# Kernel optimization log

Hardware: AMD Instinct MI355X
Metric: run time of the kernel (lower is better)

The kernel has to match this reference:

```python
import jax, jax.numpy as jnp
import numpy as np
from jax import lax

# ---- config (matches init_kwargs) ----
B, T, H = 4, 2048, 1024
HU = 4 * H                 # h_up = hidden*4
LAYERS, INDEX = 12, 0
K_CLAMP, K_EPS = 60.0, 1e-8
LN_EPS = 1e-5


def setup_inputs() -> dict:
    key = jax.random.key(0)
    ks = jax.random.split(key, 9)
    s = 0.02  # weight scale
    tr01 = INDEX / (LAYERS - 1)          # time_ratio_0_to_1
    tr1pz = 1.0 - INDEX / LAYERS         # time_ratio_1_to_pz
    i_h = np.arange(H, dtype=np.float64) / H
    i_hu = np.arange(HU, dtype=np.float64)
    # per-channel decay speed / first (sized to the WKV channel dim h_up)
    decay_speed = -5.0 + 8.0 * (i_hu / (HU - 1)) ** (0.7 + 1.3 * tr01)
    zigzag = ((np.arange(HU) + 1) % 3 - 1) * 0.5
    time_first = np.log(0.3) + zigzag
    f32 = lambda a: jnp.asarray(a, jnp.float32)
    return {
        "x": jax.random.normal(ks[0], (B, T, H), jnp.float32),
        "ln0_g": jnp.ones((H,), jnp.float32), "ln0_b": jnp.zeros((H,), jnp.float32),
        "pre_g": jnp.ones((H,), jnp.float32), "pre_b": jnp.zeros((H,), jnp.float32),
        "post_g": jnp.ones((H,), jnp.float32), "post_b": jnp.zeros((H,), jnp.float32),
        "tm_decay": f32(decay_speed),
        "tm_first": f32(time_first),
        "tm_mix_k": f32(i_h ** tr1pz),
        "tm_mix_v": f32(i_h ** tr1pz + 0.3 * tr01),
        "tm_mix_r": f32(i_h ** (0.5 * tr1pz)),
        "tm_Wk": jax.random.normal(ks[1], (H, HU), jnp.float32) * s,
        "tm_Wv": jax.random.normal(ks[2], (H, HU), jnp.float32) * s,
        "tm_Wr": jax.random.normal(ks[3], (H, HU), jnp.float32) * s,
        "tm_Wo": jax.random.normal(ks[4], (HU, H), jnp.float32) * s,
        "cm_mix_k": f32(i_h ** tr1pz),
        "cm_mix_r": f32(i_h ** tr1pz),
        "cm_Wk": jax.random.normal(ks[5], (H, HU), jnp.float32) * s,
        "cm_Wv": jax.random.normal(ks[6], (HU, H), jnp.float32) * s,
        "cm_Wr": jax.random.normal(ks[7], (H, H), jnp.float32) * s,
    }


def _ln(x, g, b):
    m = jnp.mean(x, -1, keepdims=True)
    v = jnp.mean((x - m) ** 2, -1, keepdims=True)
    return (x - m) / jnp.sqrt(v + LN_EPS) * g + b


def _shift(x):  # ZeroPad2d((0,0,1,-1)): xx[:, t] = x[:, t-1], xx[:, 0] = 0
    return jnp.pad(x[:, :-1], ((0, 0), (1, 0), (0, 0)))


def _wkv(k, kv, decay, first):
    # k, kv: [B, T, HU]; decay, first: [HU]
    # wkv[t] = first*kv[t] + sum_{d>=1} decay^(d-1) * kv[t-d]  (same for k)
    def step(carry, inp):
        sk, skv = carry
        kt, kvt = inp
        out = (first * kt + sk, first * kvt + skv)
        return (kt + decay * sk, kvt + decay * skv), out
    b = k.shape[0]
    init = (jnp.zeros((b, k.shape[2]), k.dtype), jnp.zeros((b, k.shape[2]), k.dtype))
    _, (wk, wkv) = lax.scan(step, init, (jnp.swapaxes(k, 0, 1), jnp.swapaxes(kv, 0, 1)))
    return jnp.swapaxes(wk, 0, 1), jnp.swapaxes(wkv, 0, 1)


def reference(x, ln0_g, ln0_b, pre_g, pre_b, post_g, post_b,
              tm_decay, tm_first, tm_mix_k, tm_mix_v, tm_mix_r,
              tm_Wk, tm_Wv, tm_Wr, tm_Wo,
              cm_mix_k, cm_mix_r, cm_Wk, cm_Wv, cm_Wr):
    if INDEX == 0:
        x = _ln(x, ln0_g, ln0_b)

    # ---- RWKV_TM (time mix / WKV) ----
    xn = _ln(x, pre_g, pre_b)
    xx = _shift(xn)
    xk = xn * tm_mix_k + xx * (1.0 - tm_mix_k)
    xv = xn * tm_mix_v + xx * (1.0 - tm_mix_v)
    xr = xn * tm_mix_r + xx * (1.0 - tm_mix_r)
    k = jnp.exp(jnp.minimum(xk @ tm_Wk, K_CLAMP))   # [B,T,HU]
    v = xv @ tm_Wv                                  # [B,T,HU]
    r = xr @ tm_Wr                                  # [B,T,HU]
    kv = k * v
    decay = jnp.exp(-jnp.exp(tm_decay))  # per-step multiplier exp(-exp(time_decay))
    first = jnp.exp(tm_first)
    wk, wkv = _wkv(k, kv, decay, first)
    rwkv = jax.nn.sigmoid(r) * (wkv / (wk + K_EPS))
    x = x + rwkv @ tm_Wo

    # ---- RWKV_CM (channel mix) ----
    xn = _ln(x, post_g, post_b)
    xx = _shift(xn)
    xk = xn * cm_mix_k + xx * (1.0 - cm_mix_k)
    xr = xn * cm_mix_r + xx * (1.0 - cm_mix_r)
    kv = jax.nn.silu(xk @ cm_Wk) @ cm_Wv            # [B,T,H]
    x = x + (jax.nn.sigmoid(xr @ cm_Wr) + kv)
    return x
```

## Files before the change

kernel.cpp:

```cpp
#include <hip/hip_runtime.h>

#define Hdim  1024
#define Tdim  2048
#define Bdim  4
#define HUdim 4096
#define Mrows (Bdim*Tdim)
#define CHUNK 2048
#define NCH   (HUdim/CHUNK)
#define NSEG  16
#define SEGL  (Tdim/NSEG)
#define SCHUNK 16

typedef __bf16 bf16;
typedef __bf16 bf16x2 __attribute__((ext_vector_type(2)));
typedef __bf16 bf16x8 __attribute__((ext_vector_type(8)));
typedef float  floatx4 __attribute__((ext_vector_type(4)));

__device__ __forceinline__ bf16 f2bf(float x) { return (bf16)x; }

__global__ __launch_bounds__(256) void wconv_all(
    const float* __restrict__ s0, const float* __restrict__ s1, const float* __restrict__ s2,
    const float* __restrict__ s3, const float* __restrict__ s4, const float* __restrict__ s5,
    const float* __restrict__ s6,
    bf16* d0, bf16* d1, bf16* d2, bf16* d3, bf16* d4, bf16* d5, bf16* d6) {
  __shared__ float tile[64][65];
  int bid = blockIdx.x;
  const float* src; bf16* dst; int K, N, local;
  if (bid < 1024)      { src = s0; dst = d0; K = Hdim;  N = HUdim; local = bid; }
  else if (bid < 2048) { src = s1; dst = d1; K = Hdim;  N = HUdim; local = bid - 1024; }
  else if (bid < 3072) { src = s2; dst = d2; K = Hdim;  N = HUdim; local = bid - 2048; }
  else if (bid < 4096) { src = s3; dst = d3; K = HUdim; N = Hdim;  local = bid - 3072; }
  else if (bid < 5120) { src = s4; dst = d4; K = Hdim;  N = HUdim; local = bid - 4096; }
  else if (bid < 6144) { src = s5; dst = d5; K = HUdim; N = Hdim;  local = bid - 5120; }
  else                 { src = s6; dst = d6; K = Hdim;  N = Hdim;  local = bid - 6144; }
  const int nt = N >> 6;
  const int n0 = (local % nt) * 64, k0 = (local / nt) * 64;
  const int tr = threadIdx.x >> 6;
  const int tc = threadIdx.x & 63;
#pragma unroll
  for (int j = 0; j < 16; j++) {
    int r = j * 4 + tr;
    tile[r][tc] = src[(size_t)(k0 + r) * N + n0 + tc];
  }
  __syncthreads();
#pragma unroll
  for (int j = 0; j < 16; j++) {
    int r = j * 4 + tr;
    dst[(size_t)(n0 + r) * K + k0 + tc] = f2bf(tile[tc][r]);
  }
}

__device__ __forceinline__ void block_reduce4(float v[4], float* sm) {
#pragma unroll
  for (int off = 32; off > 0; off >>= 1) {
#pragma unroll
    for (int i = 0; i < 4; i++) v[i] += __shfl_down(v[i], off, 64);
  }
  const int w = threadIdx.x >> 6;
  if ((threadIdx.x & 63) == 0) {
#pragma unroll
    for (int i = 0; i < 4; i++) sm[w * 4 + i] = v[i];
  }
  __syncthreads();
#pragma unroll
  for (int i = 0; i < 4; i++) v[i] = sm[i] + sm[4 + i] + sm[8 + i] + sm[12 + i];
  __syncthreads();
}

__global__ __launch_bounds__(256) void ln_mix_tm(
    const float* __restrict__ x,
    const float* __restrict__ g0, const float* __restrict__ b0,
    const float* __restrict__ g1, const float* __restrict__ b1,
    const float* __restrict__ mk, const float* __restrict__ mv, const float* __restrict__ mr,
    float* __restrict__ x0, bf16* __restrict__ xk, bf16* __restrict__ xv, bf16* __restrict__ xr) {
  __shared__ float sm[16];
  const int bid = blockIdx.x;
  const int t = bid & (Tdim - 1);
  const int tid = threadIdx.x;
  const bool havep = (t > 0);
  const float hp = havep ? 1.f : 0.f;
  const float* rowc = x + (size_t)bid * Hdim;
  const float* rowp = havep ? (rowc - Hdim) : rowc;

  float c[4], p[4];
#pragma unroll
  for (int j = 0; j < 4; j++) c[j] = rowc[tid * 4 + j];
#pragma unroll
  for (int j = 0; j < 4; j++) p[j] = rowp[tid * 4 + j] * hp;

  float red[4] = {0.f, 0.f, 0.f, 0.f};
#pragma unroll
  for (int j = 0; j < 4; j++) { red[0] += c[j]; red[1] += c[j]*c[j]; red[2] += p[j]; red[3] += p[j]*p[j]; }
  block_reduce4(red, sm);
  const float inv = 1.f / Hdim;
  float mc = red[0]*inv, vc = red[1]*inv - mc*mc;
  float mp = red[2]*inv, vp = red[3]*inv - mp*mp;
  float sc = rsqrtf(vc + 1e-5f), sp = rsqrtf(vp + 1e-5f);

  float yc[4], yp[4];
#pragma unroll
  for (int j = 0; j < 4; j++) {
    int i = tid * 4 + j;
    yc[j] = (c[j] - mc) * sc * g0[i] + b0[i];
    yp[j] = ((p[j] - mp) * sp * g0[i] + b0[i]) * hp;
    x0[(size_t)bid * Hdim + i] = yc[j];
  }

  float r2[4] = {0.f, 0.f, 0.f, 0.f};
#pragma unroll
  for (int j = 0; j < 4; j++) { r2[0] += yc[j]; r2[1] += yc[j]*yc[j]; r2[2] += yp[j]; r2[3] += yp[j]*yp[j]; }
  block_reduce4(r2, sm);
  float mc2 = r2[0]*inv, vc2 = r2[1]*inv - mc2*mc2;
  float mp2 = r2[2]*inv, vp2 = r2[3]*inv - mp2*mp2;
  float sc2 = rsqrtf(vc2 + 1e-5f), sp2 = rsqrtf(vp2 + 1e-5f);

#pragma unroll
  for (int j = 0; j < 4; j++) {
    int i = tid * 4 + j;
    float xnc = (yc[j] - mc2) * sc2 * g1[i] + b1[i];
    float xnp = ((yp[j] - mp2) * sp2 * g1[i] + b1[i]) * hp;
    size_t o = (size_t)bid * Hdim + i;
    float a;
    a = mk[i]; xk[o] = f2bf(xnc * a + xnp * (1.f - a));
    a = mv[i]; xv[o] = f2bf(xnc * a + xnp * (1.f - a));
    a = mr[i]; xr[o] = f2bf(xnc * a + xnp * (1.f - a));
  }
}

__global__ __launch_bounds__(256) void ln_mix_cm(
    const float* __restrict__ xin,
    const float* __restrict__ g, const float* __restrict__ bb,
    const float* __restrict__ mk, const float* __restrict__ mr,
    bf16* __restrict__ xk, bf16* __restrict__ xr) {
  __shared__ float sm[16];
  const int bid = blockIdx.x;
  const int t = bid & (Tdim - 1);
  const int tid = threadIdx.x;
  const bool havep = (t > 0);
  const float hp = havep ? 1.f : 0.f;
  const float* rowc = xin + (size_t)bid * Hdim;
  const float* rowp = havep ? (rowc - Hdim) : rowc;

  float c[4], p[4];
#pragma unroll
  for (int j = 0; j < 4; j++) c[j] = rowc[tid * 4 + j];
#pragma unroll
  for (int j = 0; j < 4; j++) p[j] = rowp[tid * 4 + j] * hp;

  float red[4] = {0.f, 0.f, 0.f, 0.f};
#pragma unroll
  for (int j = 0; j < 4; j++) { red[0] += c[j]; red[1] += c[j]*c[j]; red[2] += p[j]; red[3] += p[j]*p[j]; }
  block_reduce4(red, sm);
  const float inv = 1.f / Hdim;
  float mc = red[0]*inv, vc = red[1]*inv - mc*mc;
  float mp = red[2]*inv, vp = red[3]*inv - mp*mp;
  float sc = rsqrtf(vc + 1e-5f), sp = rsqrtf(vp + 1e-5f);

#pragma unroll
  for (int j = 0; j < 4; j++) {
    int i = tid * 4 + j;
    float xnc = (c[j] - mc) * sc * g[i] + bb[i];
    float xnp = ((p[j] - mp) * sp * g[i] + bb[i]) * hp;
    size_t o = (size_t)bid * Hdim + i;
    float a;
    a = mk[i]; xk[o] = f2bf(xnc * a + xnp * (1.f - a));
    a = mr[i]; xr[o] = f2bf(xnc * a + xnp * (1.f - a));
  }
}

__global__ __launch_bounds__(64) void wkv_part(
    const bf16* __restrict__ Kb, const bf16* __restrict__ Vb,
    float* __restrict__ stK, float* __restrict__ stKV,
    const float* __restrict__ tdec) {
  const int seg = blockIdx.x & (NSEG - 1);
  const int rest = blockIdx.x >> 4;
  const int b = rest >> 4, g = rest & 15;
  const int c = (g << 7) + (threadIdx.x << 1);
  const float d0 = __expf(-__expf(tdec[c]));
  const float d1 = __expf(-__expf(tdec[c + 1]));
  size_t base = ((size_t)b * Tdim + (size_t)seg * SEGL) * CHUNK + c;
  float sk0 = 0.f, skv0 = 0.f, sk1 = 0.f, skv1 = 0.f;
  for (int t0 = 0; t0 < SEGL; t0 += SCHUNK) {
    bf16x2 kk[SCHUNK], vv[SCHUNK];
#pragma unroll
    for (int j = 0; j < SCHUNK; j++) {
      size_t idx = base + (size_t)(t0 + j) * CHUNK;
      kk[j] = *(const bf16x2*)(Kb + idx);
      vv[j] = *(const bf16x2*)(Vb + idx);
    }
#pragma unroll
    for (int j = 0; j < SCHUNK; j++) {
      float k0 = (float)kk[j][0], k1 = (float)kk[j][1];
      float v0 = (float)vv[j][0], v1 = (float)vv[j][1];
      sk0  = fmaf(d0, sk0, k0);   skv0 = fmaf(d0, skv0, k0 * v0);
      sk1  = fmaf(d1, sk1, k1);   skv1 = fmaf(d1, skv1, k1 * v1);
    }
  }
  size_t so = ((size_t)seg * Bdim + b) * CHUNK + c;
  stK[so]      = sk0;  stK[so + 1]  = sk1;
  stKV[so]     = skv0; stKV[so + 1] = skv1;
}

__global__ __launch_bounds__(64) void wkv_emit(
    const bf16* __restrict__ Kb, const bf16* __restrict__ Vb,
    const bf16* SRb, bf16* Pb,
    const float* __restrict__ stK, const float* __restrict__ stKV,
    const float* __restrict__ tdec, const float* __restrict__ tfst) {
  const int seg = blockIdx.x & (NSEG - 1);
  const int rest = blockIdx.x >> 4;
  const int b = rest >> 4, g = rest & 15;
  const int c = (g << 7) + (threadIdx.x << 1);
  const float ed0 = __expf(tdec[c]),     ed1 = __expf(tdec[c + 1]);
  const float d0  = __expf(-ed0),        d1  = __expf(-ed1);
  const float df0 = __expf(-ed0 * (float)SEGL);
  const float df1 = __expf(-ed1 * (float)SEGL);
  const float f0  = __expf(tfst[c]),     f1  = __expf(tfst[c + 1]);

  float sk0 = 0.f, skv0 = 0.f, sk1 = 0.f, skv1 = 0.f;
  for (int j = 0; j < seg; j++) {
    size_t so = ((size_t)j * Bdim + b) * CHUNK + c;
    sk0  = fmaf(df0, sk0,  stK[so]);      sk1  = fmaf(df1, sk1,  stK[so + 1]);
    skv0 = fmaf(df0, skv0, stKV[so]);     skv1 = fmaf(df1, skv1, stKV[so + 1]);
  }

  size_t base = ((size_t)b * Tdim + (size_t)seg * SEGL) * CHUNK + c;
  for (int t0 = 0; t0 < SEGL; t0 += SCHUNK) {
    bf16x2 kk[SCHUNK], vv[SCHUNK], rr[SCHUNK];
#pragma unroll
    for (int j = 0; j < SCHUNK; j++) {
      size_t idx = base + (size_t)(t0 + j) * CHUNK;
      kk[j] = *(const bf16x2*)(Kb + idx);
      vv[j] = *(const bf16x2*)(Vb + idx);
      rr[j] = *(const bf16x2*)(SRb + idx);
    }
#pragma unroll
    for (int j = 0; j < SCHUNK; j++) {
      size_t idx = base + (size_t)(t0 + j) * CHUNK;
      float k0 = (float)kk[j][0], k1 = (float)kk[j][1];
      float v0 = (float)vv[j][0], v1 = (float)vv[j][1];
      float kv0 = k0 * v0, kv1 = k1 * v1;
      float wk0  = fmaf(f0, k0, sk0) + 1e-8f;
      float wk1  = fmaf(f1, k1, sk1) + 1e-8f;
      float wkv0 = fmaf(f0, kv0, skv0);
      float wkv1 = fmaf(f1, kv1, skv1);
      bf16x2 out;
      out[0] = f2bf((float)rr[j][0] * wkv0 * __builtin_amdgcn_rcpf(wk0));
      out[1] = f2bf((float)rr[j][1] * wkv1 * __builtin_amdgcn_rcpf(wk1));
      *(bf16x2*)(Pb + idx) = out;
      sk0  = fmaf(d0, sk0, k0);   skv0 = fmaf(d0, skv0, kv0);
      sk1  = fmaf(d1, sk1, k1);   skv1 = fmaf(d1, skv1, kv1);
    }
  }
}

__device__ __forceinline__ void gld_lds(const bf16* g, bf16* l) {
  __builtin_amdgcn_global_load_lds(
      (const __attribute__((address_space(1))) void*)(g),
      (__attribute__((address_space(3))) void*)(l),
      16, 0, 0);
}

__device__ __forceinline__ void swz(int s, int gm, int& m_t, int& n_t) {
  const int mpx  = gm >> 3;
  const int xcd  = s & 7;
  const int ss   = s >> 3;
  const int pass = mpx << 1;
  const int ng   = ss / pass;
  const int rem  = ss - ng * pass;
  m_t = xcd * mpx + (rem >> 1);
  n_t = (ng << 1) + (rem & 1);
}

__device__ __forceinline__ void mm_core64(
    const bf16* A, const bf16* Bt, int lda, int ldb, int K,
    long m0, long n0, int wv, int lane, int wm, int wn,
    bf16* As, bf16* Bs, floatx4 acc[4][4]) {
  const int srow = wv * 32 + (lane >> 2);
  const int scol = (((lane & 3) - ((lane >> 3) & 3)) & 3) * 8;
  const bf16* gA = A + (m0 + srow) * (long)lda + scol;
  const bf16* gB = Bt + (n0 + srow) * (long)ldb + scol;
  const long skipA = 16L * lda;
  const long skipB = 16L * ldb;
  bf16* lA = As + wv * 1024;
  bf16* lB = Bs + wv * 1024;
  const int pg = ((lane >> 4) + ((lane >> 1) & 3)) & 3;
  const bf16* fa = As + ((wm * 64) + (lane & 15)) * 32 + pg * 8;
  const bf16* fb = Bs + ((wn * 64) + (lane & 15)) * 32 + pg * 8;

  const int ksteps = K >> 6;
  for (int kt = 0; kt < ksteps; ++kt) {
    __syncthreads();
    gld_lds(gA, lA);             gld_lds(gA + skipA, lA + 512);
    gld_lds(gA + 32, lA + 4096); gld_lds(gA + 32 + skipA, lA + 4096 + 512);
    gld_lds(gB, lB);             gld_lds(gB + skipB, lB + 512);
    gld_lds(gB + 32, lB + 4096); gld_lds(gB + 32 + skipB, lB + 4096 + 512);
    gA += 64; gB += 64;
    __syncthreads();
#pragma unroll
    for (int s = 0; s < 2; s++) {
      bf16x8 af[4], bfr[4];
#pragma unroll
      for (int i = 0; i < 4; i++) {
        af[i]  = *(const bf16x8*)(fa + s * 4096 + i * 512);
        bfr[i] = *(const bf16x8*)(fb + s * 4096 + i * 512);
      }
#pragma unroll
      for (int mt = 0; mt < 4; mt++)
#pragma unroll
        for (int nt = 0; nt < 4; nt++)
          acc[mt][nt] = __builtin_amdgcn_mfma_f32_16x16x32_bf16(af[mt], bfr[nt], acc[mt][nt], 0, 0, 0);
    }
  }
}

enum { E_EXP = 0, E_BF16 = 1, E_SIG = 2, E_ADD1 = 3, E_SILU = 4, E_F32 = 5, E_SIGADD2 = 6 };

template <int EPI>
__device__ __forceinline__ void epilogue(
    floatx4 acc[4][4], void* Cout, const void* aux1, const void* aux2,
    long m0, long n0, int ldc, int lane, int wm, int wn) {
  const int r0 = wm * 64 + ((lane >> 4) << 2);
  const int c0 = wn * 64 + (lane & 15);
#pragma unroll
  for (int mt = 0; mt < 4; mt++) {
#pragma unroll
    for (int i = 0; i < 4; i++) {
      long r = m0 + r0 + mt * 16 + i;
      long bidx = r * (long)ldc + n0 + c0;
#pragma unroll
      for (int nt = 0; nt < 4; nt++) {
        long idx = bidx + nt * 16;
        float v = acc[mt][nt][i];
        if constexpr (EPI == E_EXP) {
          ((bf16*)Cout)[idx] = f2bf(__expf(fminf(v, 60.f)));
        } else if constexpr (EPI == E_BF16) {
          ((bf16*)Cout)[idx] = f2bf(v);
        } else if constexpr (EPI == E_SIG) {
          ((bf16*)Cout)[idx] = f2bf(1.f / (1.f + __expf(-v)));
        } else if constexpr (EPI == E_ADD1) {
          float prev = ((const float*)aux1)[idx];
          ((float*)Cout)[idx] = v + prev;
        } else if constexpr (EPI == E_SILU) {
          ((bf16*)Cout)[idx] = f2bf(v / (1.f + __expf(-v)));
        } else if constexpr (EPI == E_F32) {
          ((float*)Cout)[idx] = v;
        } else {
          float a1 = ((const float*)aux1)[idx];
          float a2 = ((const float*)aux2)[idx];
          ((float*)Cout)[idx] = a1 + 1.f / (1.f + __expf(-v)) + a2;
        }
      }
    }
  }
}

template <int EPI, int MT>
__global__ __launch_bounds__(256) void gemm_bt(
    const bf16* __restrict__ A, const bf16* __restrict__ Bt,
    void* Cout, const void* aux1, const void* aux2,
    int lda, int ldb, int ldc, int K, int gm, int gn) {
  __shared__ __align__(16) bf16 As[2 * 128 * 32];
  __shared__ __align__(16) bf16 Bs[2 * 128 * 32];
  const int tid = threadIdx.x;
  const int lane = tid & 63;
  const int wv = tid >> 6;
  const int wm = wv >> 1, wn = wv & 1;
  int m_t, n_t;
  swz(blockIdx.x, gm, m_t, n_t);
  const long n0 = (long)n_t * 128;

#pragma unroll
  for (int sm = 0; sm < MT; sm++) {
    const long m0 = (long)m_t * (128 * MT) + sm * 128;
    floatx4 acc[4][4];
#pragma unroll
    for (int i = 0; i < 4; i++)
#pragma unroll
      for (int j = 0; j < 4; j++) acc[i][j] = (floatx4){0.f, 0.f, 0.f, 0.f};
    mm_core64(A, Bt, lda, ldb, K, m0, n0, wv, lane, wm, wn, As, Bs, acc);
    epilogue<EPI>(acc, Cout, aux1, aux2, m0, n0, ldc, lane, wm, wn);
  }
}

__device__ __forceinline__ void mm_core256(
    const bf16* __restrict__ A, const bf16* __restrict__ Bt,
    int lda, int ldb, int K, long m0, long n0,
    int wv, int lane, bf16* Lds, floatx4 acc[8][4]) {
  const int wm = wv >> 2, wn = wv & 3;
  const int rA0 = wm * 128 + (wv & 3) * 16;
  const int rB0 = (wv >> 1) * 64 + (wv & 1) * 16;
  const int rl  = lane >> 2;
  const int scol = (((lane & 3) - ((lane >> 3) & 3)) & 3) * 8;
  const bf16* gA = A + (m0 + rA0 + rl) * (long)lda + scol;
  const bf16* gB = Bt + (n0 + rB0 + rl) * (long)ldb + scol;
  bf16* lA = Lds + rA0 * 32;
  bf16* lB = Lds + 16384 + rB0 * 32;

  const int pg = ((lane >> 4) + ((lane >> 1) & 3)) & 3;
  const bf16* fa0 = Lds + (wm * 128 + (lane & 15)) * 32 + pg * 8;
  const bf16* fb0 = Lds + 16384 + (wn * 64 + (lane & 15)) * 32 + pg * 8;

#define STGA8(buf, h, kt) do { \
    const bf16* _s = gA + (long)(h) * 64 * lda + (kt) * 64; \
    bf16* _d = lA + (buf) * 32768 + (h) * 2048; \
    gld_lds(_s, _d); gld_lds(_s + 32, _d + 8192); } while (0)
#define STGB8(buf, h, kt) do { \
    const bf16* _s = gB + (long)(h) * 32 * ldb + (kt) * 64; \
    bf16* _d = lB + (buf) * 32768 + (h) * 1024; \
    gld_lds(_s, _d); gld_lds(_s + 32, _d + 8192); } while (0)

  STGA8(0, 0, 0); STGB8(0, 0, 0); STGB8(0, 1, 0); STGA8(0, 1, 0);
  STGA8(1, 0, 1); STGB8(1, 0, 1); STGB8(1, 1, 1);
  asm volatile("s_waitcnt vmcnt(10)" ::: "memory");
  __builtin_amdgcn_s_barrier();

  const int niter = K >> 7;
  bf16x8 a[4][2];
  bf16x8 b[2][2][2];
  for (int it = 0; it < niter; ++it) {
    const int kt0 = it << 1;
    const bool notlast = (it != niter - 1);
#pragma unroll
    for (int ph = 0; ph < 8; ++ph) {
      const int q   = ph & 3;
      const int buf = ph >> 2;
      const int mq  = q >> 1;
      const int nq  = (q >> 1) ^ (q & 1);
      const bf16* fa = fa0 + buf * 32768 + mq * 2048;
      const bf16* fb = fb0 + buf * 32768 + nq * 1024;
      if (q == 0) {
#pragma unroll
        for (int mf = 0; mf < 4; ++mf) {
          a[mf][0] = *(const bf16x8*)(fa + mf * 512);
          a[mf][1] = *(const bf16x8*)(fa + mf * 512 + 8192);
        }
#pragma unroll
        for (int nf = 0; nf < 2; ++nf) {
          b[0][nf][0] = *(const bf16x8*)(fb + nf * 512);
          b[0][nf][1] = *(const bf16x8*)(fb + nf * 512 + 8192);
        }
      } else if (q == 1) {
#pragma unroll
        for (int nf = 0; nf < 2; ++nf) {
          b[1][nf][0] = *(const bf16x8*)(fb + nf * 512);
          b[1][nf][1] = *(const bf16x8*)(fb + nf * 512 + 8192);
        }
      } else if (q == 2) {
#pragma unroll
        for (int mf = 0; mf < 4; ++mf) {
          a[mf][0] = *(const bf16x8*)(fa + mf * 512);
          a[mf][1] = *(const bf16x8*)(fa + mf * 512 + 8192);
        }
      }
      __builtin_amdgcn_sched_barrier(0);
      if (ph == 0)            STGA8(1, 1, kt0 + 1);
      else if (notlast) {
        if (ph == 1)      STGA8(0, 0, kt0 + 2);
        else if (ph == 2) STGB8(0, 0, kt0 + 2);
        else if (ph == 3) STGB8(0, 1, kt0 + 2);
        else if (ph == 4) STGA8(0, 1, kt0 + 2);
        else if (ph == 5) STGA8(1, 0, kt0 + 3);
        else if (ph == 6) STGB8(1, 0, kt0 + 3);
        else              STGB8(1, 1, kt0 + 3);
      }
      if (notlast) {
        if (ph == 0 || ph == 1 || ph == 4 || ph == 5)
          asm volatile("s_waitcnt vmcnt(10)" ::: "memory");
        else if (ph == 3 || ph == 7)
          asm volatile("s_waitcnt vmcnt(12)" ::: "memory");
      } else {
        if (ph == 0)      asm volatile("s_waitcnt vmcnt(10)" ::: "memory");
        else if (ph == 1) asm volatile("s_waitcnt vmcnt(0)" ::: "memory");
      }
      if (q != 3) {
        __builtin_amdgcn_s_barrier();
        asm volatile("s_waitcnt lgkmcnt(0)" ::: "memory");
      }
      __builtin_amdgcn_s_setprio(1);
#pragma unroll
      for (int mf = 0; mf < 4; ++mf)
#pragma unroll
        for (int nf = 0; nf < 2; ++nf) {
          acc[mq*4+mf][nq*2+nf] = __builtin_amdgcn_mfma_f32_16x16x32_bf16(
              a[mf][0], b[nq][nf][0], acc[mq*4+mf][nq*2+nf], 0, 0, 0);
          acc[mq*4+mf][nq*2+nf] = __builtin_amdgcn_mfma_f32_16x16x32_bf16(
              a[mf][1], b[nq][nf][1], acc[mq*4+mf][nq*2+nf], 0, 0, 0);
        }
      __builtin_amdgcn_s_setprio(0);
      __builtin_amdgcn_s_barrier();
    }
  }
#undef STGA8
#undef STGB8
}

template <int EPI>
__global__ __launch_bounds__(512, 2) void gemm8(
    const bf16* __restrict__ A, const bf16* __restrict__ Bt,
    void* Cout, const void* aux1, const void* aux2,
    int lda, int ldb, int ldc, int K, int gm, int gn) {
  __shared__ __align__(16) bf16 Lds[65536];
  const int tid = threadIdx.x;
  const int lane = tid & 63;
  const int wv = tid >> 6;
  int m_t, n_t;
  swz(blockIdx.x, gm, m_t, n_t);
  const long m0 = (long)m_t * 256, n0 = (long)n_t * 256;
  floatx4 acc[8][4];
#pragma unroll
  for (int i = 0; i < 8; i++)
#pragma unroll
    for (int j = 0; j < 4; j++) acc[i][j] = (floatx4){0.f, 0.f, 0.f, 0.f};
  mm_core256(A, Bt, lda, ldb, K, m0, n0, wv, lane, Lds, acc);

  const int wm = wv >> 2, wn = wv & 3;
  const int r0 = wm * 128 + ((lane >> 4) << 2);
  const int c0 = wn * 64 + (lane & 15);
#pragma unroll
  for (int mf = 0; mf < 8; ++mf) {
#pragma unroll
    for (int i = 0; i < 4; ++i) {
      long r = m0 + r0 + mf * 16 + i;
      long bidx = r * (long)ldc + n0 + c0;
#pragma unroll
      for (int nf = 0; nf < 4; ++nf) {
        long idx = bidx + nf * 16;
        float v = acc[mf][nf][i];
        if constexpr (EPI == E_SILU) {
          ((bf16*)Cout)[idx] = f2bf(v / (1.f + __expf(-v)));
        } else if constexpr (EPI == E_BF16) {
          ((bf16*)Cout)[idx] = f2bf(v);
        } else if constexpr (EPI == E_F32) {
          ((float*)Cout)[idx] = v;
        } else if constexpr (EPI == E_ADD1) {
          float prev = ((const float*)aux1)[idx];
          ((float*)Cout)[idx] = v + prev;
        }
      }
    }
  }
}

__global__ __launch_bounds__(512, 2) void proj8(
    const bf16* __restrict__ xk, const bf16* __restrict__ xv, const bf16* __restrict__ xr,
    const bf16* __restrict__ Wk, const bf16* __restrict__ Wv, const bf16* __restrict__ Wr,
    bf16* Kc, bf16* Vc, bf16* SRc, int gm, int gn) {
  __shared__ __align__(16) bf16 Lds[65536];
  const int per = gm * gn;
  const int sub = blockIdx.x / per;
  const int s   = blockIdx.x - sub * per;
  const int tid = threadIdx.x;
  const int lane = tid & 63;
  const int wv = tid >> 6;
  int m_t, n_t;
  swz(s, gm, m_t, n_t);
  const long m0 = (long)m_t * 256, n0 = (long)n_t * 256;

  const bf16* A  = (sub == 0) ? xk : (sub == 1) ? xv : xr;
  const bf16* Bt = (sub == 0) ? Wk : (sub == 1) ? Wv : Wr;
  bf16*       C  = (sub == 0) ? Kc : (sub == 1) ? Vc : SRc;

  floatx4 acc[8][4];
#pragma unroll
  for (int i = 0; i < 8; i++)
#pragma unroll
    for (int j = 0; j < 4; j++) acc[i][j] = (floatx4){0.f, 0.f, 0.f, 0.f};
  mm_core256(A, Bt, Hdim, Hdim, Hdim, m0, n0, wv, lane, Lds, acc);

  const int wm = wv >> 2, wn = wv & 3;
  const int r0 = wm * 128 + ((lane >> 4) << 2);
  const int c0 = wn * 64 + (lane & 15);
#pragma unroll
  for (int mf = 0; mf < 8; ++mf) {
#pragma unroll
    for (int i = 0; i < 4; ++i) {
      long r = m0 + r0 + mf * 16 + i;
      long bidx = r * (long)CHUNK + n0 + c0;
#pragma unroll
      for (int nf = 0; nf < 4; ++nf) {
        long idx = bidx + nf * 16;
        float v = acc[mf][nf][i];
        float o;
        if (sub == 0)      o = __expf(fminf(v, 60.f));
        else if (sub == 1) o = v;
        else               o = 1.f / (1.f + __expf(-v));
        C[idx] = f2bf(o);
      }
    }
  }
}

extern "C" void kernel_launch(void* const* d_in, const int* in_sizes, int n_in,
                              void* d_out, int out_size, void* d_ws, size_t ws_size,
                              hipStream_t stream) {
  (void)in_sizes; (void)n_in; (void)out_size; (void)ws_size;
  const float* x        = (const float*)d_in[0];
  const float* ln0_g    = (const float*)d_in[1];
  const float* ln0_b    = (const float*)d_in[2];
  const float* pre_g    = (const float*)d_in[3];
  const float* pre_b    = (const float*)d_in[4];
  const float* post_g   = (const float*)d_in[5];
  const float* post_b   = (const float*)d_in[6];
  const float* tm_decay = (const float*)d_in[7];
  const float* tm_first = (const float*)d_in[8];
  const float* tm_mix_k = (const float*)d_in[9];
  const float* tm_mix_v = (const float*)d_in[10];
  const float* tm_mix_r = (const float*)d_in[11];
  const float* tm_Wk    = (const float*)d_in[12];
  const float* tm_Wv    = (const float*)d_in[13];
  const float* tm_Wr    = (const float*)d_in[14];
  const float* tm_Wo    = (const float*)d_in[15];
  const float* cm_mix_k = (const float*)d_in[16];
  const float* cm_mix_r = (const float*)d_in[17];
  const float* cm_Wk    = (const float*)d_in[18];
  const float* cm_Wv    = (const float*)d_in[19];
  const float* cm_Wr    = (const float*)d_in[20];

  char* ws = (char*)d_ws;
  bf16*  WkT  = (bf16*)(ws + 0);
  bf16*  WvT  = (bf16*)(ws + 8388608);
  bf16*  WrT  = (bf16*)(ws + 16777216);
  bf16*  WoT  = (bf16*)(ws + 25165824);
  bf16*  cWkT = (bf16*)(ws + 33554432);
  bf16*  cWvT = (bf16*)(ws + 41943040);
  bf16*  cWrT = (bf16*)(ws + 50331648);
  float* xres = (float*)(ws + 52428800);
  bf16*  xk   = (bf16*)(ws + 85983232);
  bf16*  xv   = (bf16*)(ws + 102760448);
  bf16*  xr   = (bf16*)(ws + 119537664);
  bf16*  Kc   = (bf16*)(ws + 136314880);
  bf16*  Vc   = (bf16*)(ws + 169869312);
  bf16*  SRc  = (bf16*)(ws + 203423744);
  float* stK  = (float*)(ws + 236978176);
  float* stKV = (float*)(ws + 237502464);
  bf16*  xk2  = (bf16*)(ws + 136314880);
  bf16*  xr2  = (bf16*)(ws + 153092096);
  bf16*  hbuf = (bf16*)(ws + 169869312);
  float* hv   = (float*)(ws + 85983232);

  dim3 blk(256);
  wconv_all<<<6400, blk, 0, stream>>>(tm_Wk, tm_Wv, tm_Wr, tm_Wo, cm_Wk, cm_Wv, cm_Wr,
                                      WkT, WvT, WrT, WoT, cWkT, cWvT, cWrT);

  ln_mix_tm<<<Mrows, blk, 0, stream>>>(x, ln0_g, ln0_b, pre_g, pre_b,
                                       tm_mix_k, tm_mix_v, tm_mix_r, xres, xk, xv, xr);

  const int scan_grid = NSEG * Bdim * (CHUNK / 128);
  const int GM = Mrows / 128;
  const int GM8 = Mrows / 256;
  const int GN8p = CHUNK / 256;
  for (int ch = 0; ch < NCH; ch++) {
    const long woff = (long)ch * CHUNK;
    proj8<<<3 * GM8 * GN8p, dim3(512), 0, stream>>>(
        xk, xv, xr, WkT + woff * Hdim, WvT + woff * Hdim, WrT + woff * Hdim,
        Kc, Vc, SRc, GM8, GN8p);

    wkv_part<<<scan_grid, dim3(64), 0, stream>>>(
        Kc, Vc, stK, stKV, tm_decay + woff);
    wkv_emit<<<scan_grid, dim3(64), 0, stream>>>(
        Kc, Vc, SRc, SRc, stK, stKV, tm_decay + woff, tm_first + woff);

    gemm_bt<E_ADD1, 1><<<GM * (Hdim/128), blk, 0, stream>>>(
        SRc, WoT + woff, xres, xres, nullptr, CHUNK, HUdim, Hdim, CHUNK, GM, Hdim/128);
  }

  ln_mix_cm<<<Mrows, blk, 0, stream>>>(xres, post_g, post_b, cm_mix_k, cm_mix_r, xk2, xr2);

  gemm8<E_SILU><<<GM8 * (HUdim/256), dim3(512), 0, stream>>>(
      xk2, cWkT, hbuf, nullptr, nullptr, Hdim, Hdim, HUdim, Hdim, GM8, HUdim/256);

  gemm_bt<E_F32, 1><<<GM * (Hdim/128), blk, 0, stream>>>(
      hbuf, cWvT, hv, nullptr, nullptr, HUdim, HUdim, Hdim, CHUNK, GM, Hdim/128);
  gemm_bt<E_ADD1, 1><<<GM * (Hdim/128), blk, 0, stream>>>(
      hbuf + CHUNK, cWvT + CHUNK, hv, hv, nullptr, HUdim, HUdim, Hdim, CHUNK, GM, Hdim/128);

  gemm_bt<E_SIGADD2, 1><<<GM * (Hdim/128), blk, 0, stream>>>(
      xr2, cWrT, (float*)d_out, xres, hv, Hdim, Hdim, Hdim, Hdim, GM, Hdim/128);
}
```

Before: 959.6 us.

## Replace 128x128 GEMMs with triple-buffered 256x128 pipelined kernel for N=1024 outputs

Replaces the single-buffered 128x128 gemm_bt kernel, which synchronizes twice per k-step, with a 512-thread 256x128 tile kernel. The new kernel triple-buffers LDS, prefetches two k-steps ahead with direct global-to-LDS loads, and raises wave priority during MFMA bursts. It also merges the two split-K cm_Wv GEMMs into one full-K launch, dropping an fp32 read-modify-write pass over hv. It uses far more LDS per block (144KB), which limits occupancy, and the grid is halved to 256 blocks for the N=1024 GEMMs.

```diff
diff --git a/kernel.cpp b/kernel.cpp
--- a/kernel.cpp
+++ b/kernel.cpp
@@ -269,48 +269,6 @@
   const int rem  = ss - ng * pass;
   m_t = xcd * mpx + (rem >> 1);
   n_t = (ng << 1) + (rem & 1);
-}
-
-__device__ __forceinline__ void mm_core64(
-    const bf16* A, const bf16* Bt, int lda, int ldb, int K,
-    long m0, long n0, int wv, int lane, int wm, int wn,
-    bf16* As, bf16* Bs, floatx4 acc[4][4]) {
-  const int srow = wv * 32 + (lane >> 2);
-  const int scol = (((lane & 3) - ((lane >> 3) & 3)) & 3) * 8;
-  const bf16* gA = A + (m0 + srow) * (long)lda + scol;
-  const bf16* gB = Bt + (n0 + srow) * (long)ldb + scol;
-  const long skipA = 16L * lda;
-  const long skipB = 16L * ldb;
-  bf16* lA = As + wv * 1024;
-  bf16* lB = Bs + wv * 1024;
-  const int pg = ((lane >> 4) + ((lane >> 1) & 3)) & 3;
-  const bf16* fa = As + ((wm * 64) + (lane & 15)) * 32 + pg * 8;
-  const bf16* fb = Bs + ((wn * 64) + (lane & 15)) * 32 + pg * 8;
-
-  const int ksteps = K >> 6;
-  for (int kt = 0; kt < ksteps; ++kt) {
-    __syncthreads();
-    gld_lds(gA, lA);             gld_lds(gA + skipA, lA + 512);
-    gld_lds(gA + 32, lA + 4096); gld_lds(gA + 32 + skipA, lA + 4096 + 512);
-    gld_lds(gB, lB);             gld_lds(gB + skipB, lB + 512);
-    gld_lds(gB + 32, lB + 4096); gld_lds(gB + 32 + skipB, lB + 4096 + 512);
-    gA += 64; gB += 64;
-    __syncthreads();
-#pragma unroll
-    for (int s = 0; s < 2; s++) {
-      bf16x8 af[4], bfr[4];
-#pragma unroll
-      for (int i = 0; i < 4; i++) {
-        af[i]  = *(const bf16x8*)(fa + s * 4096 + i * 512);
-        bfr[i] = *(const bf16x8*)(fb + s * 4096 + i * 512);
-      }
-#pragma unroll
-      for (int mt = 0; mt < 4; mt++)
-#pragma unroll
-        for (int nt = 0; nt < 4; nt++)
-          acc[mt][nt] = __builtin_amdgcn_mfma_f32_16x16x32_bf16(af[mt], bfr[nt], acc[mt][nt], 0, 0, 0);
-    }
-  }
 }
 
 enum { E_EXP = 0, E_BF16 = 1, E_SIG = 2, E_ADD1 = 3, E_SILU = 4, E_F32 = 5, E_SIGADD2 = 6 };
@@ -354,32 +312,109 @@
   }
 }
 
-template <int EPI, int MT>
-__global__ __launch_bounds__(256) void gemm_bt(
+__device__ __forceinline__ void mm_core_n128(
+    const bf16* __restrict__ A, const bf16* __restrict__ Bt,
+    int lda, int ldb, int K, long m0, long n0,
+    int wv, int lane, bf16* Lds, floatx4 acc[4][4]) {
+  const int rl  = lane >> 2;
+  const int scol = (((lane & 3) - ((lane >> 3) & 3)) & 3) * 8;
+  const bf16* gA = A + (m0 + wv * 16 + rl) * (long)lda + scol;
+  const bf16* gB = Bt + (n0 + wv * 16 + rl) * (long)ldb + scol;
+  bf16* lA = Lds + wv * 512;
+  bf16* lB = Lds + 49152 + wv * 512;
+
+  const int wm = wv >> 1, wn = wv & 1;
+  const int pg = ((lane >> 4) + ((lane >> 1) & 3)) & 3;
+  const bf16* fa0 = Lds + (wm * 64 + (lane & 15)) * 32 + pg * 8;
+  const bf16* fb0 = Lds + 49152 + (wn * 64 + (lane & 15)) * 32 + pg * 8;
+
+#define STGA_N(buf, h, kt) do { \
+    const bf16* _s = gA + (long)(h) * 128 * lda + (long)(kt) * 64; \
+    bf16* _d = lA + (buf) * 16384 + (h) * 4096; \
+    gld_lds(_s, _d); gld_lds(_s + 32, _d + 8192); } while (0)
+#define STGB_N(buf, kt) do { \
+    const bf16* _s = gB + (long)(kt) * 64; \
+    bf16* _d = lB + (buf) * 8192; \
+    gld_lds(_s, _d); gld_lds(_s + 32, _d + 4096); } while (0)
+
+  STGA_N(0, 0, 0); STGA_N(0, 1, 0); STGB_N(0, 0);
+  STGA_N(1, 0, 1); STGA_N(1, 1, 1); STGB_N(1, 1);
+  asm volatile("s_waitcnt vmcnt(6)" ::: "memory");
+  __builtin_amdgcn_s_barrier();
+
+  const int niter = K >> 6;
+  int p = 0;
+  for (int it = 0; it < niter; ++it) {
+    const int q = (p >= 1) ? p - 1 : p + 2;
+    const bool dostage = (it <= niter - 3);
+    const bf16* fa = fa0 + p * 16384;
+    const bf16* fb = fb0 + p * 8192;
+
+    bf16x8 a0[4], b0v[4];
+#pragma unroll
+    for (int i = 0; i < 4; ++i) {
+      a0[i]  = *(const bf16x8*)(fa + i * 512);
+      b0v[i] = *(const bf16x8*)(fb + i * 512);
+    }
+    __builtin_amdgcn_sched_barrier(0);
+    if (dostage) { STGA_N(q, 0, it + 2); STGA_N(q, 1, it + 2); }
+    asm volatile("s_waitcnt lgkmcnt(0)" ::: "memory");
+    __builtin_amdgcn_s_setprio(1);
+#pragma unroll
+    for (int mf = 0; mf < 4; ++mf)
+#pragma unroll
+      for (int nf = 0; nf < 4; ++nf)
+        acc[mf][nf] = __builtin_amdgcn_mfma_f32_16x16x32_bf16(a0[mf], b0v[nf], acc[mf][nf], 0, 0, 0);
+    __builtin_amdgcn_s_setprio(0);
+
+    bf16x8 a1[4], b1v[4];
+#pragma unroll
+    for (int i = 0; i < 4; ++i) {
+      a1[i]  = *(const bf16x8*)(fa + 8192 + i * 512);
+      b1v[i] = *(const bf16x8*)(fb + 4096 + i * 512);
+    }
+    __builtin_amdgcn_sched_barrier(0);
+    if (dostage) STGB_N(q, it + 2);
+    asm volatile("s_waitcnt lgkmcnt(0)" ::: "memory");
+    __builtin_amdgcn_s_setprio(1);
+#pragma unroll
+    for (int mf = 0; mf < 4; ++mf)
+#pragma unroll
+      for (int nf = 0; nf < 4; ++nf)
+        acc[mf][nf] = __builtin_amdgcn_mfma_f32_16x16x32_bf16(a1[mf], b1v[nf], acc[mf][nf], 0, 0, 0);
+    __builtin_amdgcn_s_setprio(0);
+
+    if (it < niter - 1) {
+      if (dostage) asm volatile("s_waitcnt vmcnt(6)" ::: "memory");
+      else         asm volatile("s_waitcnt vmcnt(0)" ::: "memory");
+      __builtin_amdgcn_s_barrier();
+    }
+    p = (p == 2) ? 0 : p + 1;
+  }
+#undef STGA_N
+#undef STGB_N
+}
+
+template <int EPI>
+__global__ __launch_bounds__(512, 2) void gemm8n(
     const bf16* __restrict__ A, const bf16* __restrict__ Bt,
     void* Cout, const void* aux1, const void* aux2,
     int lda, int ldb, int ldc, int K, int gm, int gn) {
-  __shared__ __align__(16) bf16 As[2 * 128 * 32];
-  __shared__ __align__(16) bf16 Bs[2 * 128 * 32];
+  __shared__ __align__(16) bf16 Lds[73728];
   const int tid = threadIdx.x;
   const int lane = tid & 63;
   const int wv = tid >> 6;
-  const int wm = wv >> 1, wn = wv & 1;
   int m_t, n_t;
   swz(blockIdx.x, gm, m_t, n_t);
-  const long n0 = (long)n_t * 128;
-
-#pragma unroll
-  for (int sm = 0; sm < MT; sm++) {
-    const long m0 = (long)m_t * (128 * MT) + sm * 128;
-    floatx4 acc[4][4];
-#pragma unroll
-    for (int i = 0; i < 4; i++)
-#pragma unroll
-      for (int j = 0; j < 4; j++) acc[i][j] = (floatx4){0.f, 0.f, 0.f, 0.f};
-    mm_core64(A, Bt, lda, ldb, K, m0, n0, wv, lane, wm, wn, As, Bs, acc);
-    epilogue<EPI>(acc, Cout, aux1, aux2, m0, n0, ldc, lane, wm, wn);
-  }
+  const long m0 = (long)m_t * 256, n0 = (long)n_t * 128;
+  floatx4 acc[4][4];
+#pragma unroll
+  for (int i = 0; i < 4; i++)
+#pragma unroll
+    for (int j = 0; j < 4; j++) acc[i][j] = (floatx4){0.f, 0.f, 0.f, 0.f};
+  mm_core_n128(A, Bt, lda, ldb, K, m0, n0, wv, lane, Lds, acc);
+  const int wm = wv >> 1, wn = wv & 1;
+  epilogue<EPI>(acc, Cout, aux1, aux2, m0, n0, ldc, lane, wm, wn);
 }
 
 __device__ __forceinline__ void mm_core256(
@@ -646,9 +681,9 @@
                                        tm_mix_k, tm_mix_v, tm_mix_r, xres, xk, xv, xr);
 
   const int scan_grid = NSEG * Bdim * (CHUNK / 128);
-  const int GM = Mrows / 128;
   const int GM8 = Mrows / 256;
   const int GN8p = CHUNK / 256;
+  const int GNn = Hdim / 128;
   for (int ch = 0; ch < NCH; ch++) {
     const long woff = (long)ch * CHUNK;
     proj8<<<3 * GM8 * GN8p, dim3(512), 0, stream>>>(
@@ -660,8 +695,8 @@
     wkv_emit<<<scan_grid, dim3(64), 0, stream>>>(
         Kc, Vc, SRc, SRc, stK, stKV, tm_decay + woff, tm_first + woff);
 
-    gemm_bt<E_ADD1, 1><<<GM * (Hdim/128), blk, 0, stream>>>(
-        SRc, WoT + woff, xres, xres, nullptr, CHUNK, HUdim, Hdim, CHUNK, GM, Hdim/128);
+    gemm8n<E_ADD1><<<GM8 * GNn, dim3(512), 0, stream>>>(
+        SRc, WoT + woff, xres, xres, nullptr, CHUNK, HUdim, Hdim, CHUNK, GM8, GNn);
   }
 
   ln_mix_cm<<<Mrows, blk, 0, stream>>>(xres, post_g, post_b, cm_mix_k, cm_mix_r, xk2, xr2);
@@ -669,11 +704,9 @@
   gemm8<E_SILU><<<GM8 * (HUdim/256), dim3(512), 0, stream>>>(
       xk2, cWkT, hbuf, nullptr, nullptr, Hdim, Hdim, HUdim, Hdim, GM8, HUdim/256);
 
-  gemm_bt<E_F32, 1><<<GM * (Hdim/128), blk, 0, stream>>>(
-      hbuf, cWvT, hv, nullptr, nullptr, HUdim, HUdim, Hdim, CHUNK, GM, Hdim/128);
-  gemm_bt<E_ADD1, 1><<<GM * (Hdim/128), blk, 0, stream>>>(
-      hbuf + CHUNK, cWvT + CHUNK, hv, hv, nullptr, HUdim, HUdim, Hdim, CHUNK, GM, Hdim/128);
-
-  gemm_bt<E_SIGADD2, 1><<<GM * (Hdim/128), blk, 0, stream>>>(
-      xr2, cWrT, (float*)d_out, xres, hv, Hdim, Hdim, Hdim, Hdim, GM, Hdim/128);
-}
+  gemm8n<E_F32><<<GM8 * GNn, dim3(512), 0, stream>>>(
+      hbuf, cWvT, hv, nullptr, nullptr, HUdim, HUdim, Hdim, HUdim, GM8, GNn);
+
+  gemm8n<E_SIGADD2><<<GM8 * GNn, dim3(512), 0, stream>>>(
+      xr2, cWrT, (float*)d_out, xres, hv, Hdim, Hdim, Hdim, Hdim, GM8, GNn);
+}
```

Result: faster. 867.5 us (-9.6%).
